# Kernel tuning notes

Hardware: AMD Instinct MI355X
Metric: run time of the kernel (lower is better)

## Reference

```python
import jax, jax.numpy as jnp
import numpy as np

K = 5            # kernel_size per pseudo-dim
N = 51200        # nodes
E = 819200       # edges (avg degree 16)
B = 64           # graphs in batch

# 2^dim corner offsets for degree-1 (linear) open B-spline in dim=2
_BITS = jnp.array([[0, 0], [0, 1], [1, 0], [1, 1]], dtype=jnp.int32)  # [4,2]

def spline_basis(pseudo):
    # pseudo: [E,2] in [0,1]. Returns basis [E,4], weight indices [E,4].
    v = pseudo * (K - 1)
    lo = jnp.clip(jnp.floor(v).astype(jnp.int32), 0, K - 2)   # [E,2]
    frac = v - lo.astype(pseudo.dtype)                        # [E,2]
    idx = lo[:, None, :] + _BITS[None]                        # [E,4,2]
    w = jnp.where(_BITS[None] == 1, frac[:, None, :], 1.0 - frac[:, None, :])
    basis = w.prod(-1)                                        # [E,4]
    widx = idx[..., 0] * K + idx[..., 1]                      # [E,4] in [0,25)
    return basis, widx

def spline_conv(x, src, dst, basis, widx, W, root, bias):
    # x:[N,Fin], W:[25,Fin,Fout], root:[Fin,Fout], bias:[Fout]
    n = x.shape[0]
    Z = jnp.einsum('ni,kio->nko', x, W)          # [N,25,Fout] per-node per-kernel transforms
    Zg = Z[src[:, None], widx]                   # [E,4,Fout] irregular gather
    msg = jnp.einsum('es,eso->eo', basis, Zg)    # [E,Fout]
    agg = jax.ops.segment_sum(msg, dst, num_segments=n)
    deg = jax.ops.segment_sum(jnp.ones_like(msg[:, 0]), dst, num_segments=n)
    agg = agg / jnp.maximum(deg, 1.0)[:, None]   # mean aggregation
    return agg + x @ root + bias

def setup_inputs():
    key = jax.random.key(0)
    ks = jax.random.split(key, 12)
    x = jax.random.normal(ks[0], (N, 7), jnp.float32)
    edge_index = jax.random.randint(ks[1], (2, E), 0, N, dtype=jnp.int32)
    pseudo = jax.random.uniform(ks[2], (E, 2), jnp.float32)
    slices = jnp.arange(B + 1, dtype=jnp.int32) * (N // B)   # graph boundaries
    W1 = jax.random.normal(ks[3], (K * K, 7, 32), jnp.float32) * 0.2
    root1 = jax.random.normal(ks[4], (7, 32), jnp.float32) * 0.2
    b1 = jnp.zeros((32,), jnp.float32)
    W2 = jax.random.normal(ks[5], (K * K, 32, 64), jnp.float32) * 0.1
    root2 = jax.random.normal(ks[6], (32, 64), jnp.float32) * 0.1
    b2 = jnp.zeros((64,), jnp.float32)
    fc_w = jax.random.normal(ks[7], (64, 30), jnp.float32) * 0.1
    fc_b = jnp.zeros((30,), jnp.float32)
    return {"x": x, "edge_index": edge_index, "pseudo": pseudo, "slices": slices,
            "W1": W1, "root1": root1, "b1": b1, "W2": W2, "root2": root2,
            "b2": b2, "fc_w": fc_w, "fc_b": fc_b}

def reference(x, edge_index, pseudo, slices, W1, root1, b1, W2, root2, b2, fc_w, fc_b):
    src, dst = edge_index[0], edge_index[1]
    basis, widx = spline_basis(pseudo)
    h = jax.nn.elu(spline_conv(x, src, dst, basis, widx, W1, root1, b1))
    h = jax.nn.elu(spline_conv(h, src, dst, basis, widx, W2, root2, b2))
    # batch_average: mean of node features per graph (slices = boundaries)
    gid = jnp.clip(jnp.searchsorted(slices, jnp.arange(N), side='right') - 1, 0, B - 1)
    sums = jax.ops.segment_sum(h, gid, num_segments=B)
    counts = (slices[1:] - slices[:-1]).astype(h.dtype)
    g = sums / jnp.maximum(counts, 1.0)[:, None]             # [B,64]
    # dropout is identity in eval mode
    logits = g @ fc_w + fc_b
    return jax.nn.log_softmax(logits, axis=-1)
```

## Files before the change

### kernel.cpp

```cpp
#include <hip/hip_runtime.h>
#include <hip/hip_fp16.h>
#include <math.h>

#define N_NODES 51200
#define N_EDGES 819200
#define NB 64
#define CAP 64

typedef _Float16 half8 __attribute__((ext_vector_type(8)));
typedef __attribute__((ext_vector_type(4))) float float4v;

__device__ __forceinline__ float eluf(float x) {
  return x > 0.f ? x : expm1f(x);
}

__device__ __forceinline__ void dec2(int w0, int w1, int c, float& basf, int& Kc) {
  int K = w0 >> 16;
  float f0 = __half2float(__ushort_as_half((unsigned short)(w1 & 0xFFFF)));
  float f1 = __half2float(__ushort_as_half((unsigned short)(((unsigned)w1) >> 16)));
  float b0 = (c & 2) ? f0 : 1.f - f0;
  float bv = (c & 1) ? f1 : 1.f - f1;
  Kc = K + (c >> 1) * 5 + (c & 1);
  basf = b0 * bv;
}

__device__ __forceinline__ void rmw16(unsigned* Tr, int Kc, int q, float bf, int4 hv) {
  __half2 bas = __float2half2_rn(bf);
  __half2* tp = (__half2*)&Tr[Kc * 16 + q * 4];
  const __half2* h = (const __half2*)&hv;
  __half2 t0 = tp[0], t1 = tp[1], t2 = tp[2], t3 = tp[3];
  tp[0] = __hfma2(bas, h[0], t0);
  tp[1] = __hfma2(bas, h[1], t1);
  tp[2] = __hfma2(bas, h[2], t2);
  tp[3] = __hfma2(bas, h[3], t3);
}

__global__ __launch_bounds__(256) void prep(const float* __restrict__ x,
                                            const float* __restrict__ W1,
                                            const float* __restrict__ root1,
                                            const float* __restrict__ W2,
                                            const float* __restrict__ root2,
                                            __half* __restrict__ xh,
                                            __half* __restrict__ W1T,
                                            __half* __restrict__ W2T,
                                            float* __restrict__ gbuf) {
  int b = blockIdx.x, tid = threadIdx.x;
  if (b < 1600) {
    int idx = b * 256 + tid;
    int n = idx >> 3, j = idx & 7;
    xh[idx] = __float2half((j < 7) ? x[n * 7 + j] : 0.f);
  } else if (b < 1628) {
    int idx = (b - 1600) * 256 + tid;
    int o = idx / 224, k = idx - o * 224;
    float v = 0.f;
    if (k < 200) {
      int cell = k >> 3, f = k & 7;
      if (f < 7) v = W1[(cell * 7 + f) * 32 + o];
    } else if (k < 207) {
      v = root1[(k - 200) * 32 + o];
    }
    W1T[idx] = __float2half(v);
  } else if (b < 1836) {
    int idx = (b - 1628) * 256 + tid;
    int o = idx / 832, k = idx - o * 832;
    float v = (k < 800) ? W2[k * 64 + o] : root2[(k - 800) * 64 + o];
    W2T[idx] = __float2half(v);
  } else {
    int idx = (b - 1836) * 256 + tid;
    gbuf[idx] = 0.f;
  }
}

__global__ __launch_bounds__(256) void scatter_eid(const int* __restrict__ ei,
                                                   const float* __restrict__ pseudo,
                                                   int* __restrict__ cnt,
                                                   int2* __restrict__ bucket) {
  int base = blockIdx.x * 2048 + threadIdx.x;
#pragma unroll
  for (int u = 0; u < 8; u++) {
    int e = base + u * 256;
    int src = ei[e], dst = ei[N_EDGES + e];
    float v0 = pseudo[2 * e] * 4.f;
    float v1 = pseudo[2 * e + 1] * 4.f;
    int lo0 = min(max((int)floorf(v0), 0), 3);
    int lo1 = min(max((int)floorf(v1), 0), 3);
    float f0 = v0 - (float)lo0, f1 = v1 - (float)lo1;
    int K = lo0 * 5 + lo1;
    unsigned short u0 = __half_as_ushort(__float2half(f0));
    unsigned short u1 = __half_as_ushort(__float2half(f1));
    int w0 = src | (K << 16);
    int w1 = (int)((unsigned)u0 | ((unsigned)u1 << 16));
    int slot = atomicAdd(&cnt[dst], 1);
    if (slot < CAP) bucket[(size_t)dst * CAP + slot] = make_int2(w0, w1);
  }
}

__global__ __launch_bounds__(256) void build_perm(const int* __restrict__ cnt,
                                                  int* __restrict__ perm) {
  __shared__ int hist[65];
  __shared__ int base_s[65];
  int g = blockIdx.x, tid = threadIdx.x;
  int n0 = g * 800;
  if (tid < 65) hist[tid] = 0;
  __syncthreads();
  for (int i = tid; i < 800; i += 256) {
    int d = min(cnt[n0 + i], 64);
    atomicAdd(&hist[d], 1);
  }
  __syncthreads();
  if (tid == 0) {
    int s = 0;
    for (int b = 0; b < 65; b++) { base_s[b] = s; s += hist[b]; }
  }
  __syncthreads();
  for (int i = tid; i < 800; i += 256) {
    int d = min(cnt[n0 + i], 64);
    int pos = atomicAdd(&base_s[d], 1);
    perm[n0 + pos] = n0 + i;
  }
}

#define L1N 16
__global__ __launch_bounds__(256) void fused_l1(const int2* __restrict__ bucket,
                                                const int* __restrict__ cnt,
                                                const int* __restrict__ perm,
                                                const unsigned* __restrict__ xh,
                                                const __half* __restrict__ W1T,
                                                const float* __restrict__ b1,
                                                unsigned short* __restrict__ h1h) {
  __shared__ unsigned T[L1N * 112];
  __shared__ float invdeg_s[L1N];
  __shared__ int pn_s[L1N];
  int tid = threadIdx.x;
  int n0 = blockIdx.x * L1N;
  for (int idx = tid; idx < L1N * 112; idx += 256) T[idx] = 0u;
  if (tid < L1N) {
    int pn = perm[n0 + tid];
    pn_s[tid] = pn;
    invdeg_s[tid] = 1.f / fmaxf((float)cnt[pn], 1.f);
  }
  __syncthreads();
  if (tid < L1N * 4) {
    int row = tid >> 2, p = tid & 3;
    int n = pn_s[row];
    float dgc = fmaxf((float)cnt[n], 1.f);
    unsigned xv = xh[n * 4 + p];
    __half2 h = __hmul2(*(const __half2*)&xv, __float2half2_rn(dgc));
    T[row * 112 + 100 + p] = *(unsigned*)&h;
  }
  int wv = tid >> 6, l = tid & 63;
  int slot = l >> 4, c = (l >> 2) & 3, p = l & 3;
  int nn = wv * 4 + slot;
  int n = pn_s[nn];
  int dg = min(cnt[n], CAP);
  int dmax = dg;
  dmax = max(dmax, __shfl_xor(dmax, 16));
  dmax = max(dmax, __shfl_xor(dmax, 32));
  const int2* bk = bucket + (size_t)n * CAP;
  unsigned* Tr = &T[nn * 112];
  int4 ra0 = *(const int4*)(bk + 0);
  int4 rb0 = *(const int4*)(bk + 2);
  int4 ra1 = *(const int4*)(bk + 4);
  int4 rb1 = *(const int4*)(bk + 6);
  unsigned xv0 = xh[(ra0.x & 0xFFFF) * 4 + p];
  unsigned xv1 = xh[(ra0.z & 0xFFFF) * 4 + p];
  unsigned xv2 = xh[(rb0.x & 0xFFFF) * 4 + p];
  unsigned xv3 = xh[(rb0.z & 0xFFFF) * 4 + p];
  for (int j = 0; j < dmax; j += 4) {
    int jp = min(j + 8, CAP - 4);
    int4 ra2 = *(const int4*)(bk + jp);
    int4 rb2 = *(const int4*)(bk + jp + 2);
    unsigned nx0 = xh[(ra1.x & 0xFFFF) * 4 + p];
    unsigned nx1 = xh[(ra1.z & 0xFFFF) * 4 + p];
    unsigned nx2 = xh[(rb1.x & 0xFFFF) * 4 + p];
    unsigned nx3 = xh[(rb1.z & 0xFFFF) * 4 + p];
    bool a0 = j < dg, a1 = j + 1 < dg, a2 = j + 2 < dg, a3 = j + 3 < dg;
    float bf; int Kc;
    if (a0) { dec2(ra0.x, ra0.y, c, bf, Kc);
      __half2* tp = (__half2*)&Tr[Kc * 4 + p];
      *tp = __hfma2(__float2half2_rn(bf), *(const __half2*)&xv0, *tp); }
    if (a1) { dec2(ra0.z, ra0.w, c, bf, Kc);
      __half2* tp = (__half2*)&Tr[Kc * 4 + p];
      *tp = __hfma2(__float2half2_rn(bf), *(const __half2*)&xv1, *tp); }
    if (a2) { dec2(rb0.x, rb0.y, c, bf, Kc);
      __half2* tp = (__half2*)&Tr[Kc * 4 + p];
      *tp = __hfma2(__float2half2_rn(bf), *(const __half2*)&xv2, *tp); }
    if (a3) { dec2(rb0.z, rb0.w, c, bf, Kc);
      __half2* tp = (__half2*)&Tr[Kc * 4 + p];
      *tp = __hfma2(__float2half2_rn(bf), *(const __half2*)&xv3, *tp); }
    ra0 = ra1; rb0 = rb1; ra1 = ra2; rb1 = rb2;
    xv0 = nx0; xv1 = nx1; xv2 = nx2; xv3 = nx3;
  }
  __syncthreads();
  if (wv < 2) {
    int m = l & 15, quad = l >> 4;
    const char* abase = (const char*)T + m * 448 + quad * 16;
    const __half* bbase = W1T + (wv * 16 + m) * 224 + quad * 8;
    float4v acc = {0.f, 0.f, 0.f, 0.f};
#pragma unroll
    for (int it = 0; it < 7; it++) {
      half8 af = *(const half8*)(abase + it * 64);
      half8 bf = *(const half8*)(bbase + it * 32);
      acc = __builtin_amdgcn_mfma_f32_16x16x32_f16(af, bf, acc, 0, 0, 0);
    }
    int feat = wv * 16 + m;
    float bb = b1[feat];
#pragma unroll
    for (int r = 0; r < 4; r++) {
      int row = quad * 4 + r;
      float v = eluf(acc[r] * invdeg_s[row] + bb);
      h1h[(size_t)pn_s[row] * 32 + feat] = __half_as_ushort(__float2half(v));
    }
  }
}

#define L2N 16
__global__ __launch_bounds__(256) void fused_l2(const int2* __restrict__ bucket,
                                                const int* __restrict__ cnt,
                                                const int* __restrict__ perm,
                                                const unsigned* __restrict__ h1hu,
                                                const __half* __restrict__ W2T,
                                                const float* __restrict__ b2,
                                                float* __restrict__ gbuf) {
  __shared__ unsigned T16[L2N * 420];
  __shared__ float invdeg_s[L2N];
  __shared__ int pn_s[L2N];
  int tid = threadIdx.x;
  int n0 = blockIdx.x * L2N;
  for (int idx = tid; idx < L2N * 420; idx += 256) T16[idx] = 0u;
  if (tid < L2N) {
    int pn = perm[n0 + tid];
    pn_s[tid] = pn;
    invdeg_s[tid] = 1.f / fmaxf((float)cnt[pn], 1.f);
  }
  __syncthreads();
  {
    int row = tid >> 4, p = tid & 15;
    int n = pn_s[row];
    float dgc = fmaxf((float)cnt[n], 1.f);
    unsigned hv = h1hu[(size_t)n * 16 + p];
    __half2 h = __hmul2(*(const __half2*)&hv, __float2half2_rn(dgc));
    T16[row * 420 + 400 + p] = *(unsigned*)&h;
  }
  int wv = tid >> 6, l = tid & 63;
  int slot = l >> 4, c = (l >> 2) & 3, q = l & 3;
  int nn = wv * 4 + slot;
  int n = pn_s[nn];
  int dg = min(cnt[n], CAP);
  int dmax = dg;
  dmax = max(dmax, __shfl_xor(dmax, 16));
  dmax = max(dmax, __shfl_xor(dmax, 32));
  const int2* bk = bucket + (size_t)n * CAP;
  unsigned* Tr = &T16[nn * 420];
  const unsigned* h1q = h1hu + q * 4;
  int4 ra0 = *(const int4*)(bk + 0);
  int4 rb0 = *(const int4*)(bk + 2);
  int4 ra1 = *(const int4*)(bk + 4);
  int4 rb1 = *(const int4*)(bk + 6);
  int4 hv0 = *(const int4*)(h1q + (size_t)(ra0.x & 0xFFFF) * 16);
  int4 hv1 = *(const int4*)(h1q + (size_t)(ra0.z & 0xFFFF) * 16);
  int4 hv2 = *(const int4*)(h1q + (size_t)(rb0.x & 0xFFFF) * 16);
  int4 hv3 = *(const int4*)(h1q + (size_t)(rb0.z & 0xFFFF) * 16);
  for (int j = 0; j < dmax; j += 4) {
    int jp = min(j + 8, CAP - 4);
    int4 ra2 = *(const int4*)(bk + jp);
    int4 rb2 = *(const int4*)(bk + jp + 2);
    int4 nh0 = *(const int4*)(h1q + (size_t)(ra1.x & 0xFFFF) * 16);
    int4 nh1 = *(const int4*)(h1q + (size_t)(ra1.z & 0xFFFF) * 16);
    int4 nh2 = *(const int4*)(h1q + (size_t)(rb1.x & 0xFFFF) * 16);
    int4 nh3 = *(const int4*)(h1q + (size_t)(rb1.z & 0xFFFF) * 16);
    bool a0 = j < dg, a1 = j + 1 < dg, a2 = j + 2 < dg, a3 = j + 3 < dg;
    float bf; int Kc;
    if (a0) { dec2(ra0.x, ra0.y, c, bf, Kc); rmw16(Tr, Kc, q, bf, hv0); }
    if (a1) { dec2(ra0.z, ra0.w, c, bf, Kc); rmw16(Tr, Kc, q, bf, hv1); }
    if (a2) { dec2(rb0.x, rb0.y, c, bf, Kc); rmw16(Tr, Kc, q, bf, hv2); }
    if (a3) { dec2(rb0.z, rb0.w, c, bf, Kc); rmw16(Tr, Kc, q, bf, hv3); }
    ra0 = ra1; rb0 = rb1; ra1 = ra2; rb1 = rb2;
    hv0 = nh0; hv1 = nh1; hv2 = nh2; hv3 = nh3;
  }
  __syncthreads();
  int m = l & 15, quad = l >> 4;
  const char* abase = (const char*)T16 + m * 1680 + quad * 16;
  const __half* bbase = W2T + (size_t)(wv * 16 + m) * 832 + quad * 8;
  float4v acc = {0.f, 0.f, 0.f, 0.f};
  for (int it = 0; it < 26; it++) {
    half8 af = *(const half8*)(abase + it * 64);
    half8 bf = *(const half8*)(bbase + it * 32);
    acc = __builtin_amdgcn_mfma_f32_16x16x32_f16(af, bf, acc, 0, 0, 0);
  }
  int feat = wv * 16 + m;
  float bb = b2[feat];
  float psum = 0.f;
#pragma unroll
  for (int r = 0; r < 4; r++) {
    int node = quad * 4 + r;
    psum += eluf(acc[r] * invdeg_s[node] + bb);
  }
  psum += __shfl_xor(psum, 16);
  psum += __shfl_xor(psum, 32);
  if (l < 16) {
    int g = n0 / 800;
    atomicAdd(&gbuf[g * 64 + feat], psum);
  }
}

__global__ __launch_bounds__(64) void fc_ls(const float* __restrict__ gbuf,
                                            const int* __restrict__ slices,
                                            const float* __restrict__ fcw,
                                            const float* __restrict__ fcb,
                                            float* __restrict__ out) {
  int g = blockIdx.x;
  int l = threadIdx.x;
  float scale = 1.f / fmaxf((float)(slices[g + 1] - slices[g]), 1.f);
  float logit = -INFINITY;
  if (l < 30) {
    float acc = fcb[l];
    for (int i = 0; i < 64; i++) acc += gbuf[g * 64 + i] * scale * fcw[i * 30 + l];
    logit = acc;
  }
  float m = logit;
  for (int off = 16; off; off >>= 1) m = fmaxf(m, __shfl_xor(m, off, 32));
  float e = (l < 30) ? expf(logit - m) : 0.f;
  for (int off = 16; off; off >>= 1) e += __shfl_xor(e, off, 32);
  if (l < 30) out[g * 30 + l] = logit - m - logf(e);
}

extern "C" void kernel_launch(void* const* d_in, const int* in_sizes, int n_in,
                              void* d_out, int out_size, void* d_ws, size_t ws_size,
                              hipStream_t stream) {
  const float* x      = (const float*)d_in[0];
  const int*   ei     = (const int*)d_in[1];
  const float* pseudo = (const float*)d_in[2];
  const int*   slices = (const int*)d_in[3];
  const float* W1     = (const float*)d_in[4];
  const float* root1  = (const float*)d_in[5];
  const float* b1     = (const float*)d_in[6];
  const float* W2     = (const float*)d_in[7];
  const float* root2  = (const float*)d_in[8];
  const float* b2     = (const float*)d_in[9];
  const float* fcw    = (const float*)d_in[10];
  const float* fcb    = (const float*)d_in[11];
  float* out = (float*)d_out;

  char* ws = (char*)d_ws;
  int*      cnt    = (int*)ws;
  int2*     bucket = (int2*)(cnt + N_NODES);
  unsigned* h1h    = (unsigned*)(bucket + (size_t)N_NODES * CAP);
  float*    gbuf   = (float*)(h1h + (size_t)N_NODES * 16);
  unsigned* xh     = (unsigned*)(gbuf + 64 * 64);
  __half*   W1T    = (__half*)(xh + (size_t)N_NODES * 4);
  __half*   W2T    = W1T + 32 * 224;
  int*      perm   = (int*)(W2T + 64 * 832);

  hipMemsetAsync(cnt, 0, N_NODES * sizeof(int), stream);

  prep<<<1852, 256, 0, stream>>>(x, W1, root1, W2, root2,
                                 (__half*)xh, W1T, W2T, gbuf);
  scatter_eid<<<N_EDGES / 2048, 256, 0, stream>>>(ei, pseudo, cnt, bucket);
  build_perm<<<NB, 256, 0, stream>>>(cnt, perm);
  fused_l1<<<N_NODES / L1N, 256, 0, stream>>>(bucket, cnt, perm, xh, W1T, b1,
                                              (unsigned short*)h1h);
  fused_l2<<<N_NODES / L2N, 256, 0, stream>>>(bucket, cnt, perm, h1h, W2T, b2,
                                              gbuf);
  fc_ls<<<NB, 64, 0, stream>>>(gbuf, slices, fcw, fcb, out);
}
```

Baseline: 211.1 us.

## Split layer-2 edge accumulation across two half-tables and split-K MFMA over 512 threads

The layer-2 fused kernel now runs with 512 threads. Each node gets two 16-lane groups that handle alternating edges, and each group accumulates into its own copy of the per-node kernel table in shared memory. The two copies are summed in fp16 just before the MFMA reduction, which is split across two wave groups along K, with partial results combined through shared memory. The goal is more parallelism and latency hiding in the gather/scatter phase. The cost is twice the shared memory per block, an extra barrier, and a simpler, shallower prefetch pipeline.

After: 235.8 us. 1.12x slower.

```diff
diff --git a/kernel.cpp b/kernel.cpp
--- a/kernel.cpp
+++ b/kernel.cpp
@@ -215,92 +215,96 @@
 }
 
 #define L2N 16
-__global__ __launch_bounds__(256) void fused_l2(const int2* __restrict__ bucket,
+__global__ __launch_bounds__(512) void fused_l2(const int2* __restrict__ bucket,
                                                 const int* __restrict__ cnt,
                                                 const int* __restrict__ perm,
                                                 const unsigned* __restrict__ h1hu,
                                                 const __half* __restrict__ W2T,
                                                 const float* __restrict__ b2,
                                                 float* __restrict__ gbuf) {
-  __shared__ unsigned T16[L2N * 420];
+  __shared__ unsigned T2[L2N * 840];
+  __shared__ float pbs[4][64][4];
   __shared__ float invdeg_s[L2N];
   __shared__ int pn_s[L2N];
   int tid = threadIdx.x;
   int n0 = blockIdx.x * L2N;
-  for (int idx = tid; idx < L2N * 420; idx += 256) T16[idx] = 0u;
+  for (int idx = tid; idx < L2N * 840; idx += 512) T2[idx] = 0u;
   if (tid < L2N) {
     int pn = perm[n0 + tid];
     pn_s[tid] = pn;
     invdeg_s[tid] = 1.f / fmaxf((float)cnt[pn], 1.f);
   }
   __syncthreads();
-  {
+  if (tid < 256) {
     int row = tid >> 4, p = tid & 15;
     int n = pn_s[row];
     float dgc = fmaxf((float)cnt[n], 1.f);
     unsigned hv = h1hu[(size_t)n * 16 + p];
     __half2 h = __hmul2(*(const __half2*)&hv, __float2half2_rn(dgc));
-    T16[row * 420 + 400 + p] = *(unsigned*)&h;
+    T2[row * 840 + 400 + p] = *(unsigned*)&h;
   }
   int wv = tid >> 6, l = tid & 63;
-  int slot = l >> 4, c = (l >> 2) & 3, q = l & 3;
-  int nn = wv * 4 + slot;
+  int nh = l >> 5, s = (l >> 4) & 1, c = (l >> 2) & 3, q = l & 3;
+  int nn = wv * 2 + nh;
   int n = pn_s[nn];
   int dg = min(cnt[n], CAP);
-  int dmax = dg;
-  dmax = max(dmax, __shfl_xor(dmax, 16));
-  dmax = max(dmax, __shfl_xor(dmax, 32));
+  int dmax = max(dg, __shfl_xor(dg, 32));
+  int iters = (dmax + 1) >> 1;
   const int2* bk = bucket + (size_t)n * CAP;
-  unsigned* Tr = &T16[nn * 420];
+  unsigned* Tr = &T2[nn * 840 + s * 420];
   const unsigned* h1q = h1hu + q * 4;
-  int4 ra0 = *(const int4*)(bk + 0);
-  int4 rb0 = *(const int4*)(bk + 2);
-  int4 ra1 = *(const int4*)(bk + 4);
-  int4 rb1 = *(const int4*)(bk + 6);
-  int4 hv0 = *(const int4*)(h1q + (size_t)(ra0.x & 0xFFFF) * 16);
-  int4 hv1 = *(const int4*)(h1q + (size_t)(ra0.z & 0xFFFF) * 16);
-  int4 hv2 = *(const int4*)(h1q + (size_t)(rb0.x & 0xFFFF) * 16);
-  int4 hv3 = *(const int4*)(h1q + (size_t)(rb0.z & 0xFFFF) * 16);
-  for (int j = 0; j < dmax; j += 4) {
-    int jp = min(j + 8, CAP - 4);
-    int4 ra2 = *(const int4*)(bk + jp);
-    int4 rb2 = *(const int4*)(bk + jp + 2);
-    int4 nh0 = *(const int4*)(h1q + (size_t)(ra1.x & 0xFFFF) * 16);
-    int4 nh1 = *(const int4*)(h1q + (size_t)(ra1.z & 0xFFFF) * 16);
-    int4 nh2 = *(const int4*)(h1q + (size_t)(rb1.x & 0xFFFF) * 16);
-    int4 nh3 = *(const int4*)(h1q + (size_t)(rb1.z & 0xFFFF) * 16);
-    bool a0 = j < dg, a1 = j + 1 < dg, a2 = j + 2 < dg, a3 = j + 3 < dg;
-    float bf; int Kc;
-    if (a0) { dec2(ra0.x, ra0.y, c, bf, Kc); rmw16(Tr, Kc, q, bf, hv0); }
-    if (a1) { dec2(ra0.z, ra0.w, c, bf, Kc); rmw16(Tr, Kc, q, bf, hv1); }
-    if (a2) { dec2(rb0.x, rb0.y, c, bf, Kc); rmw16(Tr, Kc, q, bf, hv2); }
-    if (a3) { dec2(rb0.z, rb0.w, c, bf, Kc); rmw16(Tr, Kc, q, bf, hv3); }
-    ra0 = ra1; rb0 = rb1; ra1 = ra2; rb1 = rb2;
-    hv0 = nh0; hv1 = nh1; hv2 = nh2; hv3 = nh3;
+  int2 rec0 = bk[s];
+  int2 rec1 = bk[2 + s];
+  int4 hv0 = *(const int4*)(h1q + (size_t)(rec0.x & 0xFFFF) * 16);
+  for (int t = 0; t < iters; t++) {
+    int2 rec2 = bk[min(2 * t + 4 + s, 63)];
+    int4 hv1 = *(const int4*)(h1q + (size_t)(rec1.x & 0xFFFF) * 16);
+    if (2 * t + s < dg) {
+      float bf; int Kc;
+      dec2(rec0.x, rec0.y, c, bf, Kc);
+      rmw16(Tr, Kc, q, bf, hv0);
+    }
+    rec0 = rec1; rec1 = rec2; hv0 = hv1;
   }
   __syncthreads();
   int m = l & 15, quad = l >> 4;
-  const char* abase = (const char*)T16 + m * 1680 + quad * 16;
-  const __half* bbase = W2T + (size_t)(wv * 16 + m) * 832 + quad * 8;
+  int f = wv & 3, kh = wv >> 2;
+  const char* a0 = (const char*)T2 + m * 3360 + quad * 16;
+  const __half* bbase = W2T + (size_t)(f * 16 + m) * 832 + quad * 8;
   float4v acc = {0.f, 0.f, 0.f, 0.f};
-  for (int it = 0; it < 26; it++) {
-    half8 af = *(const half8*)(abase + it * 64);
+  for (int it = kh * 13; it < kh * 13 + 13; it++) {
+    half8 afa = *(const half8*)(a0 + it * 64);
+    half8 afb = *(const half8*)(a0 + 1680 + it * 64);
+    __half2* pa = (__half2*)&afa;
+    const __half2* pb = (const __half2*)&afb;
+    pa[0] = __hadd2(pa[0], pb[0]);
+    pa[1] = __hadd2(pa[1], pb[1]);
+    pa[2] = __hadd2(pa[2], pb[2]);
+    pa[3] = __hadd2(pa[3], pb[3]);
     half8 bf = *(const half8*)(bbase + it * 32);
-    acc = __builtin_amdgcn_mfma_f32_16x16x32_f16(af, bf, acc, 0, 0, 0);
-  }
-  int feat = wv * 16 + m;
-  float bb = b2[feat];
-  float psum = 0.f;
+    acc = __builtin_amdgcn_mfma_f32_16x16x32_f16(afa, bf, acc, 0, 0, 0);
+  }
+  if (kh == 1) {
+    pbs[f][l][0] = acc[0]; pbs[f][l][1] = acc[1];
+    pbs[f][l][2] = acc[2]; pbs[f][l][3] = acc[3];
+  }
+  __syncthreads();
+  if (kh == 0) {
+    int feat = f * 16 + m;
+    float bb = b2[feat];
+    float psum = 0.f;
 #pragma unroll
-  for (int r = 0; r < 4; r++) {
-    int node = quad * 4 + r;
-    psum += eluf(acc[r] * invdeg_s[node] + bb);
-  }
-  psum += __shfl_xor(psum, 16);
-  psum += __shfl_xor(psum, 32);
-  if (l < 16) {
-    int g = n0 / 800;
-    atomicAdd(&gbuf[g * 64 + feat], psum);
+    for (int r = 0; r < 4; r++) {
+      int node = quad * 4 + r;
+      float v = acc[r] + pbs[f][l][r];
+      psum += eluf(v * invdeg_s[node] + bb);
+    }
+    psum += __shfl_xor(psum, 16);
+    psum += __shfl_xor(psum, 32);
+    if (l < 16) {
+      int g = n0 / 800;
+      atomicAdd(&gbuf[g * 64 + feat], psum);
+    }
   }
 }
 
@@ -360,7 +364,7 @@
   build_perm<<<NB, 256, 0, stream>>>(cnt, perm);
   fused_l1<<<N_NODES / L1N, 256, 0, stream>>>(bucket, cnt, perm, xh, W1T, b1,
                                               (unsigned short*)h1h);
-  fused_l2<<<N_NODES / L2N, 256, 0, stream>>>(bucket, cnt, perm, h1h, W2T, b2,
+  fused_l2<<<N_NODES / L2N, 512, 0, stream>>>(bucket, cnt, perm, h1h, W2T, b2,
                                               gbuf);
   fc_ls<<<NB, 64, 0, stream>>>(gbuf, slices, fcw, fcb, out);
 }
```
